# Kernel tuning notes

Measured on AMD Instinct MI355X. Metric: run time of the kernel, lower is better.

Reference implementation:

```python
import jax, jax.numpy as jnp
import numpy as np

B, S, IK, IV = 16, 2048, 3, 1
D = IK + IV          # input_size = 4
H = 256              # hidden_size
F = 512              # dim_feedforward
L = 2                # num_layers
EPS = 1e-5


def setup_inputs() -> dict:
    key = jax.random.key(0)
    ks = jax.random.split(key, 16)
    n = jax.random.normal
    inp = {
        'KEY': n(ks[0], (B, S, IK), jnp.float32),
        'VALUE': n(ks[1], (B, S, IV), jnp.float32),
        # per-layer kernel-attention projections (stacked on layer axis)
        'Wq': n(ks[2], (L, D, H), jnp.float32) * 0.1,
        'bq': jnp.zeros((L, H), jnp.float32),
        'Wk': n(ks[3], (L, D, H), jnp.float32) * 0.1,
        'bk': jnp.zeros((L, H), jnp.float32),
        'Wv': n(ks[4], (L, D, H), jnp.float32) * 0.1,
        'bv': jnp.zeros((L, H), jnp.float32),
        'Wo': n(ks[5], (L, H, D), jnp.float32) * 0.1,
        'bo': jnp.zeros((L, D), jnp.float32),
        'bw': jnp.ones((L,), jnp.float32),          # Gaussian kernel bandwidth
        # LayerNorm 1
        'g1': jnp.ones((L, D), jnp.float32),
        'be1': jnp.zeros((L, D), jnp.float32),
        # FFN
        'W1': n(ks[6], (L, D, F), jnp.float32) * 0.1,
        'b1': jnp.zeros((L, F), jnp.float32),
        'W2': n(ks[7], (L, F, D), jnp.float32) * 0.1,
        'b2': jnp.zeros((L, D), jnp.float32),
        # LayerNorm 2
        'g2': jnp.ones((L, D), jnp.float32),
        'be2': jnp.zeros((L, D), jnp.float32),
        # final fc: input_size -> input_v
        'Wfc': n(ks[8], (D, IV), jnp.float32) * 0.1,
        'bfc': jnp.zeros((IV,), jnp.float32),
    }
    return inp


def _layernorm(x, g, b):
    m = x.mean(-1, keepdims=True)
    v = ((x - m) ** 2).mean(-1, keepdims=True)
    return (x - m) * jax.lax.rsqrt(v + EPS) * g + b


def reference(KEY, VALUE, Wq, bq, Wk, bk, Wv, bv, Wo, bo, bw,
              g1, be1, W1, b1, W2, b2, g2, be2, Wfc, bfc):
    # positioning: concat coords and values -> [B, S, D]
    X = jnp.concatenate([KEY, VALUE], axis=-1)
    n_layers = Wq.shape[0]
    for i in range(n_layers):
        # Nadaraya-Watson Gaussian kernel attention (madsnn, type='nwd', kernel='gauss')
        Q = X @ Wq[i] + bq[i]                      # [B,S,H]
        K = X @ Wk[i] + bk[i]                      # [B,S,H]
        V = X @ Wv[i] + bv[i]                      # [B,S,H]
        # pairwise squared distances ||q-k||^2, [B,S,S]
        d2 = ((Q * Q).sum(-1)[:, :, None]
              + (K * K).sum(-1)[:, None, :]
              - 2.0 * jnp.einsum('bqh,bkh->bqk', Q, K))
        attn = jax.nn.softmax(-0.5 * d2 * (bw[i] ** 2), axis=-1)
        attn_out = jnp.einsum('bqk,bkh->bqh', attn, V) @ Wo[i] + bo[i]  # [B,S,D]
        # residual + LayerNorm + FFN + residual + LayerNorm (dropout = identity in eval)
        res = _layernorm(X + attn_out, g1[i], be1[i])
        ff = jax.nn.relu(res @ W1[i] + b1[i]) @ W2[i] + b2[i]
        X = _layernorm(res + ff, g2[i], be2[i])
    return X @ Wfc + bfc                            # [B,S,IV]
```

## Files before the change

kernel.cpp:

```cpp
#include <hip/hip_runtime.h>

#define BB 16
#define SS 2048
#define NTOK (BB*SS)
#define FF 512
#define EPSF 1e-5f

#if __has_builtin(__builtin_amdgcn_exp2f)
#define EXP2F(x) __builtin_amdgcn_exp2f(x)
#else
#define EXP2F(x) exp2f(x)
#endif


__device__ __forceinline__ float wred64(float v) {
#pragma unroll
  for (int m = 32; m > 0; m >>= 1) v += __shfl_xor(v, m, 64);
  return v;
}


__global__ __launch_bounds__(256) void prep_kernel(
    const float* __restrict__ KEY, const float* __restrict__ VALUE,
    const float* __restrict__ Wq, const float* __restrict__ bq,
    const float* __restrict__ Wk, const float* __restrict__ bk,
    const float* __restrict__ Wv, const float* __restrict__ bv,
    const float* __restrict__ Wo, const float* __restrict__ bw,
    const float* __restrict__ W1, const float* __restrict__ b1,
    const float* __restrict__ W2,
    float* __restrict__ sm, float* __restrict__ w1t, float* __restrict__ X0)
{
  const int bid = blockIdx.x;
  if (bid < 128) {
    const int gq = bid*256 + threadIdx.x;
    *(float4*)(X0 + (size_t)gq*4) =
        make_float4(KEY[gq*3 + 0], KEY[gq*3 + 1], KEY[gq*3 + 2], VALUE[gq]);
    return;
  }
  const int i = bid - 128;
  if (threadIdx.x >= 64) return;
  const int lane = threadIdx.x;
  float m4[4][4] = {{0}}, gkk[4][4] = {{0}}, wvo[4][4] = {{0}};
  float akk[4] = {0}, bvo[4] = {0};
  float ck1 = 0.f, ck2 = 0.f;

  for (int h = lane; h < 256; h += 64) {
    float vq[4], vk[4], vv[4], wo4[4];
#pragma unroll
    for (int a = 0; a < 4; ++a) {
      vq[a]  = Wq[(i*4 + a)*256 + h];
      vk[a]  = Wk[(i*4 + a)*256 + h];
      vv[a]  = Wv[(i*4 + a)*256 + h];
      wo4[a] = Wo[(i*256 + h)*4 + a];
    }
    const float bqh = bq[i*256 + h], bkh = bk[i*256 + h], bvh = bv[i*256 + h];
#pragma unroll
    for (int a = 0; a < 4; ++a) {
#pragma unroll
      for (int c = 0; c < 4; ++c) {
        m4[a][c]  = fmaf(vq[a], vk[c], m4[a][c]);
        gkk[a][c] = fmaf(vk[a], vk[c], gkk[a][c]);
        wvo[a][c] = fmaf(vv[a], wo4[c], wvo[a][c]);
      }
      akk[a] = fmaf(vk[a], bqh - bkh, akk[a]);
      bvo[a] = fmaf(bvh, wo4[a], bvo[a]);
    }
    ck1 = fmaf(bqh, bkh, ck1);
    ck2 = fmaf(bkh, bkh, ck2);
  }
#pragma unroll
  for (int a = 0; a < 4; ++a) {
#pragma unroll
    for (int c = 0; c < 4; ++c) {
      m4[a][c]  = wred64(m4[a][c]);
      gkk[a][c] = wred64(gkk[a][c]);
      wvo[a][c] = wred64(wvo[a][c]);
    }
    akk[a] = wred64(akk[a]);
    bvo[a] = wred64(bvo[a]);
  }
  ck1 = wred64(ck1); ck2 = wred64(ck2);

  if (lane == 0) {
    const float bwv = bw[i];
    const float bw2 = bwv * bwv * 1.44269504088896f;
    float* s = sm + i*64;
#pragma unroll
    for (int a = 0; a < 4; ++a) {
#pragma unroll
      for (int c = 0; c < 4; ++c) {
        s[a*4+c]      = bw2 * m4[a][c];
        s[16 + a*4+c] = -0.5f * bw2 * gkk[a][c];
        s[32 + a*4+c] = wvo[a][c];
      }
      s[48+a] = bw2 * akk[a];
      s[52+a] = bvo[a];
    }
    s[56] = bw2 * (ck1 - 0.5f * ck2);
  }
  for (int f = lane; f < FF; f += 64) {
    float* rec = w1t + (i*FF + f)*12;
#pragma unroll
    for (int c = 0; c < 4; ++c) rec[c]   = W1[(i*4 + c)*FF + f];
#pragma unroll
    for (int c = 0; c < 4; ++c) rec[4+c] = W2[(i*FF + f)*4 + c];
    rec[8] = b1[i*FF + f];
    rec[9] = 0.f; rec[10] = 0.f; rec[11] = 0.f;
  }
}

__device__ __forceinline__ void compute_feat(const float x[4], const float* __restrict__ s,
                                             float* __restrict__ featrec)
{
  float P[4], VT[4], tk[4];
#pragma unroll
  for (int a = 0; a < 4; ++a) {
    P[a]  = fmaf(s[a*4+3], x[3], fmaf(s[a*4+2], x[2], fmaf(s[a*4+1], x[1], s[a*4+0]*x[0])));
    tk[a] = fmaf(s[16+a*4+3], x[3], fmaf(s[16+a*4+2], x[2], fmaf(s[16+a*4+1], x[1], s[16+a*4+0]*x[0])));
    VT[a] = s[52+a] + fmaf(s[32+3*4+a], x[3], fmaf(s[32+2*4+a], x[2], fmaf(s[32+1*4+a], x[1], s[32+0*4+a]*x[0])));
  }
  float R = s[56];
#pragma unroll
  for (int a = 0; a < 4; ++a) R = fmaf(tk[a] + s[48+a], x[a], R);
  float4* fp = (float4*)featrec;
  fp[0] = make_float4(P[0], P[1], P[2], P[3]);
  fp[1] = make_float4(VT[0], VT[1], VT[2], VT[3]);
  fp[2] = make_float4(R, 0.f, 0.f, 0.f);
}

__global__ __launch_bounds__(256) void attn_kernel(
    const float* __restrict__ X, const float* __restrict__ sm,
    float* __restrict__ part)
{
  __shared__ float smem[512*21];
  const int bid = blockIdx.x;
  const int b = bid >> 5;
  const int r = bid & 31;
  const int qg = r >> 3, kb = r & 7;
  const int qbase = (b << 11) + (qg << 9);
  const int kbase = (b << 11) + (kb << 8);
  const int tid = threadIdx.x;
  const int lane = tid & 63, wave = tid >> 6;

  {
    const float4 xk = *(const float4*)(X + (size_t)(kbase + tid)*4);
    float xr[4] = {xk.x, xk.y, xk.z, xk.w};
    float fr[12];
    compute_feat(xr, sm, fr);
    float* dst = smem + tid*12;
    ((float4*)dst)[0] = ((float4*)fr)[0];
    ((float4*)dst)[1] = ((float4*)fr)[1];
    dst[8] = fr[8];
  }

  float xq[8][4], acc[8][5];
#pragma unroll
  for (int j = 0; j < 8; ++j) {
    const float4 xv = *(const float4*)(X + (size_t)(qbase + j*64 + lane)*4);
    xq[j][0] = xv.x; xq[j][1] = xv.y; xq[j][2] = xv.z; xq[j][3] = xv.w;
#pragma unroll
    for (int c = 0; c < 5; ++c) acc[j][c] = 0.f;
  }
  __syncthreads();

  const float* kf = smem + wave*64*12;
#pragma unroll 2
  for (int k = 0; k < 64; ++k) {
    const float* kp = kf + k*12;
    const float4 P  = *(const float4*)kp;
    const float4 VT = *(const float4*)(kp + 4);
    const float R = kp[8];
#pragma unroll
    for (int j = 0; j < 8; ++j) {
      float l = fmaf(xq[j][3], P.w, fmaf(xq[j][2], P.z,
                fmaf(xq[j][1], P.y, fmaf(xq[j][0], P.x, R))));
      const float e = EXP2F(l);
      acc[j][0] = fmaf(e, VT.x, acc[j][0]);
      acc[j][1] = fmaf(e, VT.y, acc[j][1]);
      acc[j][2] = fmaf(e, VT.z, acc[j][2]);
      acc[j][3] = fmaf(e, VT.w, acc[j][3]);
      acc[j][4] += e;
    }
  }
  __syncthreads();
#pragma unroll
  for (int j = 0; j < 8; ++j) {
    float* rr = smem + (j*64 + lane)*21 + wave*5;
    rr[0] = acc[j][0]; rr[1] = acc[j][1]; rr[2] = acc[j][2];
    rr[3] = acc[j][3]; rr[4] = acc[j][4];
  }
  __syncthreads();
  float* pb = part + (size_t)kb * NTOK * 8;
#pragma unroll
  for (int t = 0; t < 2; ++t) {
    const int q = t*256 + tid;
    const float* rr = smem + q*21;
    float s0 = 0.f, s1 = 0.f, s2 = 0.f, s3 = 0.f, s4 = 0.f;
#pragma unroll
    for (int w = 0; w < 4; ++w) {
      s0 += rr[w*5+0]; s1 += rr[w*5+1]; s2 += rr[w*5+2];
      s3 += rr[w*5+3]; s4 += rr[w*5+4];
    }
    float* pp = pb + (size_t)(qbase + q)*8;
    *(float4*)pp = make_float4(s0, s1, s2, s3);
    pp[4] = s4;
  }
}

__device__ __forceinline__ void ln4(const float t[4], const float* __restrict__ g,
                                    const float* __restrict__ b, float r[4])
{
  const float m = 0.25f*(t[0]+t[1]+t[2]+t[3]);
  const float d0 = t[0]-m, d1 = t[1]-m, d2 = t[2]-m, d3 = t[3]-m;
  const float v = 0.25f*(d0*d0 + d1*d1 + d2*d2 + d3*d3);
  const float sc = rsqrtf(v + EPSF);
  r[0] = fmaf(d0*sc, g[0], b[0]);
  r[1] = fmaf(d1*sc, g[1], b[1]);
  r[2] = fmaf(d2*sc, g[2], b[2]);
  r[3] = fmaf(d3*sc, g[3], b[3]);
}

__global__ __launch_bounds__(512) void combine_kernel(
    const float* __restrict__ part, const float* __restrict__ Xin,
    const float* __restrict__ w1t,
    const float* __restrict__ bo, const float* __restrict__ g1, const float* __restrict__ be1,
    const float* __restrict__ b2v, const float* __restrict__ g2, const float* __restrict__ be2,
    float* __restrict__ Xout,
    const float* __restrict__ Wfc, const float* __restrict__ bfc,
    float* __restrict__ outp, int last)
{
  const int tok = threadIdx.x & 63, fc = threadIdx.x >> 6;
  const int gq = blockIdx.x*64 + tok;
  __shared__ float redp[8][64][5];
  __shared__ float ress[64][4];
  __shared__ float redf[8][64][4];

  {
    const float* pp = part + ((size_t)fc*NTOK + gq)*8;
    const float4 v = *(const float4*)pp;
    redp[fc][tok][0] = v.x; redp[fc][tok][1] = v.y;
    redp[fc][tok][2] = v.z; redp[fc][tok][3] = v.w;
    redp[fc][tok][4] = pp[4];
  }
  __syncthreads();

  if (fc == 0) {
    float acc[5] = {0,0,0,0,0};
#pragma unroll
    for (int k = 0; k < 8; ++k)
#pragma unroll
      for (int c = 0; c < 5; ++c) acc[c] += redp[k][tok][c];
    const float inv = 1.0f / acc[4];
    const float4 xv = *(const float4*)(Xin + (size_t)gq*4);
    float t[4];
    t[0] = xv.x + fmaf(acc[0], inv, bo[0]);
    t[1] = xv.y + fmaf(acc[1], inv, bo[1]);
    t[2] = xv.z + fmaf(acc[2], inv, bo[2]);
    t[3] = xv.w + fmaf(acc[3], inv, bo[3]);
    float r[4];
    ln4(t, g1, be1, r);
    ress[tok][0] = r[0]; ress[tok][1] = r[1]; ress[tok][2] = r[2]; ress[tok][3] = r[3];
  }
  __syncthreads();

  const float r0 = ress[tok][0], r1 = ress[tok][1], r2 = ress[tok][2], r3 = ress[tok][3];
  float fa[4] = {0,0,0,0};
  const float* wt = w1t + (size_t)fc*64*12;
#pragma unroll 4
  for (int f = 0; f < 64; ++f) {
    const float* rec = wt + f*12;
    const float4 w1r = *(const float4*)rec;
    const float4 w2r = *(const float4*)(rec + 4);
    const float b1f = rec[8];
    float h = fmaf(r3, w1r.w, fmaf(r2, w1r.z, fmaf(r1, w1r.y, fmaf(r0, w1r.x, b1f))));
    h = fmaxf(h, 0.f);
    fa[0] = fmaf(h, w2r.x, fa[0]);
    fa[1] = fmaf(h, w2r.y, fa[1]);
    fa[2] = fmaf(h, w2r.z, fa[2]);
    fa[3] = fmaf(h, w2r.w, fa[3]);
  }
  redf[fc][tok][0] = fa[0]; redf[fc][tok][1] = fa[1];
  redf[fc][tok][2] = fa[2]; redf[fc][tok][3] = fa[3];
  __syncthreads();

  if (fc == 0) {
    float t2[4];
#pragma unroll
    for (int c = 0; c < 4; ++c) {
      float s = b2v[c];
#pragma unroll
      for (int k = 0; k < 8; ++k) s += redf[k][tok][c];
      t2[c] = ress[tok][c] + s;
    }
    float y[4];
    ln4(t2, g2, be2, y);
    if (last) {
      outp[gq] = fmaf(y[3], Wfc[3], fmaf(y[2], Wfc[2], fmaf(y[1], Wfc[1], fmaf(y[0], Wfc[0], bfc[0]))));
    } else {
      *(float4*)(Xout + (size_t)gq*4) = make_float4(y[0], y[1], y[2], y[3]);
    }
  }
}

extern "C" void kernel_launch(void* const* d_in, const int* in_sizes, int n_in,
                              void* d_out, int out_size, void* d_ws, size_t ws_size,
                              hipStream_t stream)
{
  const float* KEY   = (const float*)d_in[0];
  const float* VALUE = (const float*)d_in[1];
  const float* Wq  = (const float*)d_in[2];
  const float* bq  = (const float*)d_in[3];
  const float* Wk  = (const float*)d_in[4];
  const float* bk  = (const float*)d_in[5];
  const float* Wv  = (const float*)d_in[6];
  const float* bv  = (const float*)d_in[7];
  const float* Wo  = (const float*)d_in[8];
  const float* bo  = (const float*)d_in[9];
  const float* bw  = (const float*)d_in[10];
  const float* g1  = (const float*)d_in[11];
  const float* be1 = (const float*)d_in[12];
  const float* W1  = (const float*)d_in[13];
  const float* b1  = (const float*)d_in[14];
  const float* W2  = (const float*)d_in[15];
  const float* b2  = (const float*)d_in[16];
  const float* g2  = (const float*)d_in[17];
  const float* be2 = (const float*)d_in[18];
  const float* Wfc = (const float*)d_in[19];
  const float* bfc = (const float*)d_in[20];
  float* out = (float*)d_out;

  float* w    = (float*)d_ws;
  float* sm   = w;
  float* w1t  = w + 128;
  float* X0   = w + 12416;
  float* X1   = w + 143488;
  float* part = w + 274560;

  prep_kernel<<<130, 256, 0, stream>>>(KEY, VALUE, Wq, bq, Wk, bk, Wv, bv, Wo, bw,
                                       W1, b1, W2, sm, w1t, X0);

  attn_kernel<<<512, 256, 0, stream>>>(X0, sm, part);
  combine_kernel<<<512, 512, 0, stream>>>(part, X0, w1t,
      bo, g1, be1, b2, g2, be2,
      X1, Wfc, bfc, out, 0);

  attn_kernel<<<512, 256, 0, stream>>>(X1, sm + 64, part);
  combine_kernel<<<512, 512, 0, stream>>>(part, X1, w1t + FF*12,
      bo + 4, g1 + 4, be1 + 4, b2 + 4, g2 + 4, be2 + 4,
      X0, Wfc, bfc, out, 1);
}
```

Baseline: 186.8 us.

## Fold prep kernel into attention and combine kernels, dropping a launch

Removes the separate prep kernel. Each attention block now recomputes the per-layer folded 4x4 attention matrices from Wq/Wk/Wv/Wo using wave reductions and shared memory. Layer 0 reads KEY/VALUE directly instead of a concatenated X0 buffer, and the FFN reads W1/b1/W2 directly rather than a repacked record. This saves one launch and an extra pass over the token data, at the cost of redundant per-block weight reductions and less contiguous weight loads in the FFN loop.

```diff
diff --git a/kernel.cpp b/kernel.cpp
--- a/kernel.cpp
+++ b/kernel.cpp
@@ -20,96 +20,7 @@
 }
 
 
-__global__ __launch_bounds__(256) void prep_kernel(
-    const float* __restrict__ KEY, const float* __restrict__ VALUE,
-    const float* __restrict__ Wq, const float* __restrict__ bq,
-    const float* __restrict__ Wk, const float* __restrict__ bk,
-    const float* __restrict__ Wv, const float* __restrict__ bv,
-    const float* __restrict__ Wo, const float* __restrict__ bw,
-    const float* __restrict__ W1, const float* __restrict__ b1,
-    const float* __restrict__ W2,
-    float* __restrict__ sm, float* __restrict__ w1t, float* __restrict__ X0)
-{
-  const int bid = blockIdx.x;
-  if (bid < 128) {
-    const int gq = bid*256 + threadIdx.x;
-    *(float4*)(X0 + (size_t)gq*4) =
-        make_float4(KEY[gq*3 + 0], KEY[gq*3 + 1], KEY[gq*3 + 2], VALUE[gq]);
-    return;
-  }
-  const int i = bid - 128;
-  if (threadIdx.x >= 64) return;
-  const int lane = threadIdx.x;
-  float m4[4][4] = {{0}}, gkk[4][4] = {{0}}, wvo[4][4] = {{0}};
-  float akk[4] = {0}, bvo[4] = {0};
-  float ck1 = 0.f, ck2 = 0.f;
-
-  for (int h = lane; h < 256; h += 64) {
-    float vq[4], vk[4], vv[4], wo4[4];
-#pragma unroll
-    for (int a = 0; a < 4; ++a) {
-      vq[a]  = Wq[(i*4 + a)*256 + h];
-      vk[a]  = Wk[(i*4 + a)*256 + h];
-      vv[a]  = Wv[(i*4 + a)*256 + h];
-      wo4[a] = Wo[(i*256 + h)*4 + a];
-    }
-    const float bqh = bq[i*256 + h], bkh = bk[i*256 + h], bvh = bv[i*256 + h];
-#pragma unroll
-    for (int a = 0; a < 4; ++a) {
-#pragma unroll
-      for (int c = 0; c < 4; ++c) {
-        m4[a][c]  = fmaf(vq[a], vk[c], m4[a][c]);
-        gkk[a][c] = fmaf(vk[a], vk[c], gkk[a][c]);
-        wvo[a][c] = fmaf(vv[a], wo4[c], wvo[a][c]);
-      }
-      akk[a] = fmaf(vk[a], bqh - bkh, akk[a]);
-      bvo[a] = fmaf(bvh, wo4[a], bvo[a]);
-    }
-    ck1 = fmaf(bqh, bkh, ck1);
-    ck2 = fmaf(bkh, bkh, ck2);
-  }
-#pragma unroll
-  for (int a = 0; a < 4; ++a) {
-#pragma unroll
-    for (int c = 0; c < 4; ++c) {
-      m4[a][c]  = wred64(m4[a][c]);
-      gkk[a][c] = wred64(gkk[a][c]);
-      wvo[a][c] = wred64(wvo[a][c]);
-    }
-    akk[a] = wred64(akk[a]);
-    bvo[a] = wred64(bvo[a]);
-  }
-  ck1 = wred64(ck1); ck2 = wred64(ck2);
-
-  if (lane == 0) {
-    const float bwv = bw[i];
-    const float bw2 = bwv * bwv * 1.44269504088896f;
-    float* s = sm + i*64;
-#pragma unroll
-    for (int a = 0; a < 4; ++a) {
-#pragma unroll
-      for (int c = 0; c < 4; ++c) {
-        s[a*4+c]      = bw2 * m4[a][c];
-        s[16 + a*4+c] = -0.5f * bw2 * gkk[a][c];
-        s[32 + a*4+c] = wvo[a][c];
-      }
-      s[48+a] = bw2 * akk[a];
-      s[52+a] = bvo[a];
-    }
-    s[56] = bw2 * (ck1 - 0.5f * ck2);
-  }
-  for (int f = lane; f < FF; f += 64) {
-    float* rec = w1t + (i*FF + f)*12;
-#pragma unroll
-    for (int c = 0; c < 4; ++c) rec[c]   = W1[(i*4 + c)*FF + f];
-#pragma unroll
-    for (int c = 0; c < 4; ++c) rec[4+c] = W2[(i*FF + f)*4 + c];
-    rec[8] = b1[i*FF + f];
-    rec[9] = 0.f; rec[10] = 0.f; rec[11] = 0.f;
-  }
-}
-
-__device__ __forceinline__ void compute_feat(const float x[4], const float* __restrict__ s,
+__device__ __forceinline__ void compute_feat(const float x[4], const float* s,
                                              float* __restrict__ featrec)
 {
   float P[4], VT[4], tk[4];
@@ -129,10 +40,17 @@
 }
 
 __global__ __launch_bounds__(256) void attn_kernel(
-    const float* __restrict__ X, const float* __restrict__ sm,
-    float* __restrict__ part)
+    const float* __restrict__ KEY, const float* __restrict__ VALUE,
+    const float* __restrict__ X,
+    const float* __restrict__ Wq, const float* __restrict__ bq,
+    const float* __restrict__ Wk, const float* __restrict__ bk,
+    const float* __restrict__ Wv, const float* __restrict__ bv,
+    const float* __restrict__ Wo, const float* __restrict__ bw,
+    float* __restrict__ part, int layer0)
 {
   __shared__ float smem[512*21];
+  __shared__ float scratch[4*58];
+  __shared__ float smL[64];
   const int bid = blockIdx.x;
   const int b = bid >> 5;
   const int r = bid & 31;
@@ -143,10 +61,70 @@
   const int lane = tid & 63, wave = tid >> 6;
 
   {
-    const float4 xk = *(const float4*)(X + (size_t)(kbase + tid)*4);
-    float xr[4] = {xk.x, xk.y, xk.z, xk.w};
+    const int h = tid;
+    float vq[4], vk[4], vv[4], wo4[4];
+#pragma unroll
+    for (int a = 0; a < 4; ++a) {
+      vq[a]  = Wq[a*256 + h];
+      vk[a]  = Wk[a*256 + h];
+      vv[a]  = Wv[a*256 + h];
+      wo4[a] = Wo[h*4 + a];
+    }
+    const float bqh = bq[h], bkh = bk[h], bvh = bv[h];
+    float p[58];
+#pragma unroll
+    for (int a = 0; a < 4; ++a)
+#pragma unroll
+      for (int c = 0; c < 4; ++c) {
+        p[a*4+c]      = vq[a] * vk[c];
+        p[16 + a*4+c] = vk[a] * vk[c];
+        p[32 + a*4+c] = vv[a] * wo4[c];
+      }
+#pragma unroll
+    for (int a = 0; a < 4; ++a) {
+      p[48+a] = vk[a] * (bqh - bkh);
+      p[52+a] = bvh * wo4[a];
+    }
+    p[56] = bqh * bkh;
+    p[57] = bkh * bkh;
+#pragma unroll
+    for (int t = 0; t < 58; ++t) p[t] = wred64(p[t]);
+    if (lane == 0) {
+#pragma unroll
+      for (int t = 0; t < 58; ++t) scratch[wave*58 + t] = p[t];
+    }
+  }
+  __syncthreads();
+  if (tid < 57) {
+    const float bwv = bw[0];
+    const float bw2 = bwv * bwv * 1.44269504088896f;
+    const float raw = scratch[tid] + scratch[58 + tid] + scratch[116 + tid] + scratch[174 + tid];
+    float v;
+    if (tid < 16)      v = bw2 * raw;
+    else if (tid < 32) v = -0.5f * bw2 * raw;
+    else if (tid < 48) v = raw;
+    else if (tid < 52) v = bw2 * raw;
+    else if (tid < 56) v = raw;
+    else {
+      const float raw57 = scratch[57] + scratch[115] + scratch[173] + scratch[231];
+      v = bw2 * (raw - 0.5f * raw57);
+    }
+    smL[tid] = v;
+  }
+  __syncthreads();
+
+  {
+    const int gk = kbase + tid;
+    float xr[4];
+    if (layer0) {
+      xr[0] = KEY[gk*3 + 0]; xr[1] = KEY[gk*3 + 1]; xr[2] = KEY[gk*3 + 2];
+      xr[3] = VALUE[gk];
+    } else {
+      const float4 xk = *(const float4*)(X + (size_t)gk*4);
+      xr[0] = xk.x; xr[1] = xk.y; xr[2] = xk.z; xr[3] = xk.w;
+    }
     float fr[12];
-    compute_feat(xr, sm, fr);
+    compute_feat(xr, smL, fr);
     float* dst = smem + tid*12;
     ((float4*)dst)[0] = ((float4*)fr)[0];
     ((float4*)dst)[1] = ((float4*)fr)[1];
@@ -156,8 +134,14 @@
   float xq[8][4], acc[8][5];
 #pragma unroll
   for (int j = 0; j < 8; ++j) {
-    const float4 xv = *(const float4*)(X + (size_t)(qbase + j*64 + lane)*4);
-    xq[j][0] = xv.x; xq[j][1] = xv.y; xq[j][2] = xv.z; xq[j][3] = xv.w;
+    const int gq = qbase + j*64 + lane;
+    if (layer0) {
+      xq[j][0] = KEY[gq*3 + 0]; xq[j][1] = KEY[gq*3 + 1]; xq[j][2] = KEY[gq*3 + 2];
+      xq[j][3] = VALUE[gq];
+    } else {
+      const float4 xv = *(const float4*)(X + (size_t)gq*4);
+      xq[j][0] = xv.x; xq[j][1] = xv.y; xq[j][2] = xv.z; xq[j][3] = xv.w;
+    }
 #pragma unroll
     for (int c = 0; c < 5; ++c) acc[j][c] = 0.f;
   }
@@ -221,13 +205,16 @@
 }
 
 __global__ __launch_bounds__(512) void combine_kernel(
-    const float* __restrict__ part, const float* __restrict__ Xin,
-    const float* __restrict__ w1t,
+    const float* __restrict__ part,
+    const float* __restrict__ KEY, const float* __restrict__ VALUE,
+    const float* __restrict__ Xin,
+    const float* __restrict__ W1, const float* __restrict__ b1,
+    const float* __restrict__ W2,
     const float* __restrict__ bo, const float* __restrict__ g1, const float* __restrict__ be1,
     const float* __restrict__ b2v, const float* __restrict__ g2, const float* __restrict__ be2,
     float* __restrict__ Xout,
     const float* __restrict__ Wfc, const float* __restrict__ bfc,
-    float* __restrict__ outp, int last)
+    float* __restrict__ outp, int layer0, int last)
 {
   const int tok = threadIdx.x & 63, fc = threadIdx.x >> 6;
   const int gq = blockIdx.x*64 + tok;
@@ -251,12 +238,19 @@
 #pragma unroll
       for (int c = 0; c < 5; ++c) acc[c] += redp[k][tok][c];
     const float inv = 1.0f / acc[4];
-    const float4 xv = *(const float4*)(Xin + (size_t)gq*4);
+    float xv[4];
+    if (layer0) {
+      xv[0] = KEY[gq*3 + 0]; xv[1] = KEY[gq*3 + 1]; xv[2] = KEY[gq*3 + 2];
+      xv[3] = VALUE[gq];
+    } else {
+      const float4 x4 = *(const float4*)(Xin + (size_t)gq*4);
+      xv[0] = x4.x; xv[1] = x4.y; xv[2] = x4.z; xv[3] = x4.w;
+    }
     float t[4];
-    t[0] = xv.x + fmaf(acc[0], inv, bo[0]);
-    t[1] = xv.y + fmaf(acc[1], inv, bo[1]);
-    t[2] = xv.z + fmaf(acc[2], inv, bo[2]);
-    t[3] = xv.w + fmaf(acc[3], inv, bo[3]);
+    t[0] = xv[0] + fmaf(acc[0], inv, bo[0]);
+    t[1] = xv[1] + fmaf(acc[1], inv, bo[1]);
+    t[2] = xv[2] + fmaf(acc[2], inv, bo[2]);
+    t[3] = xv[3] + fmaf(acc[3], inv, bo[3]);
     float r[4];
     ln4(t, g1, be1, r);
     ress[tok][0] = r[0]; ress[tok][1] = r[1]; ress[tok][2] = r[2]; ress[tok][3] = r[3];
@@ -265,14 +259,15 @@
 
   const float r0 = ress[tok][0], r1 = ress[tok][1], r2 = ress[tok][2], r3 = ress[tok][3];
   float fa[4] = {0,0,0,0};
-  const float* wt = w1t + (size_t)fc*64*12;
+  const int fbase = fc*64;
 #pragma unroll 4
-  for (int f = 0; f < 64; ++f) {
-    const float* rec = wt + f*12;
-    const float4 w1r = *(const float4*)rec;
-    const float4 w2r = *(const float4*)(rec + 4);
-    const float b1f = rec[8];
-    float h = fmaf(r3, w1r.w, fmaf(r2, w1r.z, fmaf(r1, w1r.y, fmaf(r0, w1r.x, b1f))));
+  for (int f0 = 0; f0 < 64; ++f0) {
+    const int f = fbase + f0;
+    const float w10 = W1[0*FF + f], w11 = W1[1*FF + f],
+                w12 = W1[2*FF + f], w13 = W1[3*FF + f];
+    const float4 w2r = *(const float4*)(W2 + (size_t)f*4);
+    const float b1f = b1[f];
+    float h = fmaf(r3, w13, fmaf(r2, w12, fmaf(r1, w11, fmaf(r0, w10, b1f))));
     h = fmaxf(h, 0.f);
     fa[0] = fmaf(h, w2r.x, fa[0]);
     fa[1] = fmaf(h, w2r.y, fa[1]);
@@ -330,22 +325,19 @@
   float* out = (float*)d_out;
 
   float* w    = (float*)d_ws;
-  float* sm   = w;
-  float* w1t  = w + 128;
-  float* X0   = w + 12416;
-  float* X1   = w + 143488;
-  float* part = w + 274560;
-
-  prep_kernel<<<130, 256, 0, stream>>>(KEY, VALUE, Wq, bq, Wk, bk, Wv, bv, Wo, bw,
-                                       W1, b1, W2, sm, w1t, X0);
-
-  attn_kernel<<<512, 256, 0, stream>>>(X0, sm, part);
-  combine_kernel<<<512, 512, 0, stream>>>(part, X0, w1t,
-      bo, g1, be1, b2, g2, be2,
-      X1, Wfc, bfc, out, 0);
-
-  attn_kernel<<<512, 256, 0, stream>>>(X1, sm + 64, part);
-  combine_kernel<<<512, 512, 0, stream>>>(part, X1, w1t + FF*12,
-      bo + 4, g1 + 4, be1 + 4, b2 + 4, g2 + 4, be2 + 4,
-      X0, Wfc, bfc, out, 1);
-}
+  float* X1   = w;
+  float* part = w + 131072;
+
+  attn_kernel<<<512, 256, 0, stream>>>(KEY, VALUE, nullptr,
+      Wq, bq, Wk, bk, Wv, bv, Wo, bw, part, 1);
+  combine_kernel<<<512, 512, 0, stream>>>(part, KEY, VALUE, nullptr,
+      W1, b1, W2, bo, g1, be1, b2, g2, be2,
+      X1, Wfc, bfc, out, 1, 0);
+
+  attn_kernel<<<512, 256, 0, stream>>>(KEY, VALUE, X1,
+      Wq + 1024, bq + 256, Wk + 1024, bk + 256, Wv + 1024, bv + 256,
+      Wo + 1024, bw + 1, part, 0);
+  combine_kernel<<<512, 512, 0, stream>>>(part, KEY, VALUE, X1,
+      W1 + 2048, b1 + FF, W2 + 2048, bo + 4, g1 + 4, be1 + 4, b2 + 4, g2 + 4, be2 + 4,
+      nullptr, Wfc, bfc, out, 0, 1);
+}
```

Result: slower. 193.2 us (+3.4%).
